# Kernel tuning notes

Measured on AMD Instinct MI355X. Metric: run time of the kernel, lower is better.

The kernel has to match this reference:

```python
import jax, jax.numpy as jnp
import numpy as np

H = 8          # num_heads
CHUNK = 68     # tokens_per_chunk = blocks_per_chunk(4) * tokens_per_block(17)
EPS = 1e-5


def _layer_norm(t, w, b):
    m = t.mean(-1, keepdims=True)
    v = t.var(-1, keepdims=True)
    return (t - m) / jnp.sqrt(v + EPS) * w + b


def _forward(tokens, embedding, Wq, bq, Wk, bk, Wv, bv, Wg, bg, Wo, bo,
             gn_w, gn_b, ln1_w, ln1_b, ln2_w, ln2_b, w1, b1, w2, b2):
    B, S = tokens.shape
    L, D, _ = Wq.shape
    dh = D // H
    n_chunks = S // CHUNK

    x = embedding[tokens]  # [B,S,D]

    # per-head decay gammas (standard RetNet)
    gamma = 1.0 - 2.0 ** (-5.0 - jnp.arange(H, dtype=jnp.float32))  # [H]

    # rotary relative-position tables (absolute positions, fresh state n=0)
    pos = jnp.arange(S, dtype=jnp.float32)
    inv = 1.0 / (10000.0 ** (jnp.arange(0, dh, 2, dtype=jnp.float32) / dh))
    ang = pos[:, None] * inv[None, :]                      # [S, dh/2]
    cs = jnp.concatenate([jnp.cos(ang)] * 2, -1)[None, :, None, :]  # [1,S,1,dh]
    sn = jnp.concatenate([jnp.sin(ang)] * 2, -1)[None, :, None, :]

    def rot(t):  # t: [B,S,H,dh]
        t1, t2 = jnp.split(t, 2, axis=-1)
        return t * cs + jnp.concatenate([-t2, t1], -1) * sn

    # chunkwise decay structures
    idx = jnp.arange(CHUNK, dtype=jnp.float32)
    expo = idx[:, None] - idx[None, :]
    Dmask = jnp.where(expo >= 0, gamma[:, None, None] ** expo[None], 0.0)  # [H,C,C]
    cross_dec = gamma[None, :] ** (idx[:, None] + 1.0)          # [C,H]
    k_dec = gamma[None, :] ** (CHUNK - 1.0 - idx[:, None])      # [C,H]
    chunk_dec = gamma ** CHUNK                                  # [H]

    for l in range(L):
        h = _layer_norm(x, ln1_w[l], ln1_b[l])
        q = rot((h @ Wq[l] + bq[l]).reshape(B, S, H, dh))
        k = rot((h @ Wk[l] + bk[l]).reshape(B, S, H, dh)) * (dh ** -0.5)
        v = (h @ Wv[l] + bv[l]).reshape(B, S, H, dh)
        # split into chunks, scan carries the per-head KV state [B,H,dh,dh]
        qc = q.reshape(B, n_chunks, CHUNK, H, dh).transpose(1, 0, 2, 3, 4)
        kc = k.reshape(B, n_chunks, CHUNK, H, dh).transpose(1, 0, 2, 3, 4)
        vc = v.reshape(B, n_chunks, CHUNK, H, dh).transpose(1, 0, 2, 3, 4)

        def step(state, qkv):
            qq, kk, vv = qkv  # each [B,C,H,dh]
            inner = jnp.einsum('bihd,bjhd->bhij', qq, kk) * Dmask
            out = jnp.einsum('bhij,bjhd->bihd', inner, vv)
            out = out + jnp.einsum('bihd,bhde->bihe', qq, state) * cross_dec[None, :, :, None]
            state = state * chunk_dec[None, :, None, None] + \
                jnp.einsum('bjhd,bjhe->bhde', kk * k_dec[None, :, :, None], vv)
            return state, out

        state0 = jnp.zeros((B, H, dh, dh), dtype=x.dtype)
        _, ret = jax.lax.scan(step, state0, (qc, kc, vc))
        ret = ret.transpose(1, 0, 2, 3, 4).reshape(B, S, H, dh)
        # per-head group norm
        m = ret.mean(-1, keepdims=True)
        vr = ret.var(-1, keepdims=True)
        ret = (ret - m) / jnp.sqrt(vr + EPS)
        ret = (ret * gn_w[l].reshape(H, dh) + gn_b[l].reshape(H, dh)).reshape(B, S, D)
        g = jax.nn.silu(h @ Wg[l] + bg[l])
        x = x + (g * ret) @ Wo[l] + bo[l]
        h2 = _layer_norm(x, ln2_w[l], ln2_b[l])
        x = x + jax.nn.silu(h2 @ w1[l] + b1[l]) @ w2[l] + b2[l]
    return x


def setup_inputs() -> dict:
    key = jax.random.key(0)
    B, S, D, L, FF, V = 16, 408, 512, 10, 2048, 519
    ks = jax.random.split(key, 16)
    r = lambda i, shape, s=0.02: jax.random.normal(ks[i], shape, dtype=jnp.float32) * s
    return {
        'tokens': jax.random.randint(ks[0], (B, S), 0, V, dtype=jnp.int32),
        'embedding': r(1, (V, D)),
        'Wq': r(2, (L, D, D)), 'bq': jnp.zeros((L, D), jnp.float32),
        'Wk': r(3, (L, D, D)), 'bk': jnp.zeros((L, D), jnp.float32),
        'Wv': r(4, (L, D, D)), 'bv': jnp.zeros((L, D), jnp.float32),
        'Wg': r(5, (L, D, D)), 'bg': jnp.zeros((L, D), jnp.float32),
        'Wo': r(6, (L, D, D)), 'bo': jnp.zeros((L, D), jnp.float32),
        'gn_w': jnp.ones((L, D), jnp.float32), 'gn_b': jnp.zeros((L, D), jnp.float32),
        'ln1_w': jnp.ones((L, D), jnp.float32), 'ln1_b': jnp.zeros((L, D), jnp.float32),
        'ln2_w': jnp.ones((L, D), jnp.float32), 'ln2_b': jnp.zeros((L, D), jnp.float32),
        'w1': r(7, (L, D, FF)), 'b1': jnp.zeros((L, FF), jnp.float32),
        'w2': r(8, (L, FF, D)), 'b2': jnp.zeros((L, D), jnp.float32),
    }


def reference(tokens, embedding, Wq, bq, Wk, bk, Wv, bv, Wg, bg, Wo, bo,
              gn_w, gn_b, ln1_w, ln1_b, ln2_w, ln2_b, w1, b1, w2, b2):
    return _forward(tokens, embedding, Wq, bq, Wk, bk, Wv, bv, Wg, bg, Wo, bo,
                    gn_w, gn_b, ln1_w, ln1_b, ln2_w, ln2_b, w1, b1, w2, b2)
```

## Files before the change

### kernel.cpp

```cpp
#include <hip/hip_runtime.h>
#include <hip/hip_bf16.h>

#define H 8
#define DH 64
#define DMODEL 512
#define SEQ 408
#define BATCH 16
#define NLAYER 10
#define FFDIM 2048
#define CHUNK 68
#define NCHUNK 6
#define M (BATCH*SEQ)
#define EPS 1e-5f

typedef __hip_bfloat16 bf16;
typedef unsigned short ushort_t;
typedef short bf8v __attribute__((ext_vector_type(8)));
typedef float f4v  __attribute__((ext_vector_type(4)));

static constexpr size_t QKVG_STRIDE = 2u*512*512;
static constexpr size_t QKVG_HL     = 512*512;
static constexpr size_t WO_HI = 0;
static constexpr size_t WO_LO = WO_HI + 512*512;
static constexpr size_t W1_HI = WO_LO + 512*512;
static constexpr size_t W1_LO = W1_HI + 2048*512;
static constexpr size_t W2_HI = W1_LO + 2048*512;
static constexpr size_t W2_LO = W2_HI + 512*2048;

__device__ __forceinline__ float us2f(unsigned short u){ return __uint_as_float(((unsigned)u) << 16); }
__device__ __forceinline__ unsigned short f2bfs(float f){
  __bf16 h = (__bf16)f;
  return *(unsigned short*)&h;
}
__device__ __forceinline__ void split2(float f, unsigned short& hi, unsigned short& lo){
  hi = f2bfs(f);
  lo = f2bfs(f - us2f(hi));
}

typedef const __attribute__((address_space(1))) unsigned int* gas_ptr;
typedef __attribute__((address_space(3))) unsigned int* las_ptr;
__device__ __forceinline__ void gld16(const void* g, void* l){
  __builtin_amdgcn_global_load_lds((gas_ptr)g, (las_ptr)l, 16, 0, 0);
}

__device__ __forceinline__ int xcd_swz(int fid, int nwg){
  int q = nwg >> 3;
  return (fid & 7) * q + (fid >> 3);
}

__global__ void embed_kernel(const int* __restrict__ tokens, const float* __restrict__ emb,
                             float* __restrict__ x){
  int idx = blockIdx.x*256 + threadIdx.x;
  if (idx >= M*DMODEL) return;
  int r = idx >> 9; int d = idx & 511;
  x[idx] = emb[(size_t)tokens[r]*DMODEL + d];
}

__global__ __launch_bounds__(256) void ln_kernel(const float* __restrict__ x,
    const float* __restrict__ w, const float* __restrict__ b,
    ushort_t* __restrict__ hhi, ushort_t* __restrict__ hlo){
  __shared__ float red[8];
  int r = blockIdx.x, tid = threadIdx.x;
  size_t base = (size_t)r*DMODEL;
  float v0 = x[base + tid], v1 = x[base + tid + 256];
  float s = v0 + v1, s2 = v0*v0 + v1*v1;
  int lane = tid & 63, wv = tid >> 6;
  #pragma unroll
  for (int o = 32; o; o >>= 1){ s += __shfl_xor(s, o); s2 += __shfl_xor(s2, o); }
  if (lane == 0){ red[wv] = s; red[wv+4] = s2; }
  __syncthreads();
  float tot  = red[0]+red[1]+red[2]+red[3];
  float tot2 = red[4]+red[5]+red[6]+red[7];
  float mean = tot * (1.0f/512.0f);
  float var  = tot2 * (1.0f/512.0f) - mean*mean;
  float rinv = rsqrtf(var + EPS);
  float o0 = (v0-mean)*rinv*w[tid]     + b[tid];
  float o1 = (v1-mean)*rinv*w[tid+256] + b[tid+256];
  unsigned short hi, lo;
  split2(o0, hi, lo); hhi[base+tid] = hi; hlo[base+tid] = lo;
  split2(o1, hi, lo); hhi[base+tid+256] = hi; hlo[base+tid+256] = lo;
}

__device__ __forceinline__ void wsplit_tile(const float* __restrict__ W,
    ushort_t* __restrict__ hi, ushort_t* __restrict__ lo,
    int N, int K, int n0, int k0)
{
  __shared__ float tb[32][33];
  int tx = threadIdx.x & 31, ty = threadIdx.x >> 5;
  #pragma unroll
  for (int r = 0; r < 32; r += 8)
    tb[ty+r][tx] = W[(size_t)(k0+ty+r)*N + n0 + tx];
  __syncthreads();
  #pragma unroll
  for (int r = 0; r < 32; r += 8){
    float v = tb[tx][ty+r];
    unsigned short h, l; split2(v, h, l);
    size_t o = (size_t)(n0+ty+r)*K + k0 + tx;
    hi[o] = h; lo[o] = l;
  }
}

__global__ __launch_bounds__(256) void wsplit_qkvg_kernel(
    const float* __restrict__ Wq, const float* __restrict__ Wk,
    const float* __restrict__ Wv, const float* __restrict__ Wg,
    ushort_t* __restrict__ wsp)
{
  int z = blockIdx.z;
  const float* W = (z==0)?Wq:(z==1)?Wk:(z==2)?Wv:Wg;
  ushort_t* hi = wsp + (size_t)z*QKVG_STRIDE;
  wsplit_tile(W, hi, hi + QKVG_HL, 512, 512, blockIdx.x*32, blockIdx.y*32);
}

__global__ __launch_bounds__(256) void wsplit_ffo_kernel(
    const float* __restrict__ Wo, const float* __restrict__ w1,
    const float* __restrict__ w2, ushort_t* __restrict__ wsp)
{
  int b = blockIdx.x;
  const float* W; ushort_t* hi; int N, K, n0, k0;
  if (b < 256){
    W = Wo; hi = wsp + WO_HI; N = 512; K = 512;
    n0 = (b & 15)*32; k0 = (b >> 4)*32;
  } else if (b < 1280){
    int bb = b - 256;
    W = w1; hi = wsp + W1_HI; N = 2048; K = 512;
    n0 = (bb & 63)*32; k0 = (bb >> 6)*32;
  } else {
    int bb = b - 1280;
    W = w2; hi = wsp + W2_HI; N = 512; K = 2048;
    n0 = (bb & 15)*32; k0 = (bb >> 4)*32;
  }
  wsplit_tile(W, hi, hi + (size_t)N*K, N, K, n0, k0);
}

#define BK 32

template<int TBN>
__global__ __launch_bounds__(256) void gemm_ps_kernel(
    const ushort_t* __restrict__ Ahi, const ushort_t* __restrict__ Alo,
    const ushort_t* __restrict__ Bhi, const ushort_t* __restrict__ Blo,
    const float* __restrict__ bias,
    const float* Cin, float* Cout, ushort_t* Co_hi, ushort_t* Co_lo,
    int N, int K, int epi)
{
  constexpr int TNW = TBN/32;
  __shared__ __align__(16) short AsH[2][64*BK];
  __shared__ __align__(16) short AsL[2][64*BK];
  __shared__ __align__(16) short BsH[2][TBN*BK];
  __shared__ __align__(16) short BsL[2][TBN*BK];
  int tid = threadIdx.x;
  int lane = tid & 63, wave = tid >> 6;
  int wm = (wave >> 1) * 32, wn = (wave & 1) * (TBN/2);
  int l15 = lane & 15, quad = lane >> 4;

  int nwg = gridDim.x * gridDim.y;
  int fid = blockIdx.y * gridDim.x + blockIdx.x;
  int swz = xcd_swz(fid, nwg);
  int bn = (swz % gridDim.x) * TBN;
  int bm = (swz / gridDim.x) * 64;

  f4v acc[2][TNW];
  #pragma unroll
  for (int i = 0; i < 2; i++)
    #pragma unroll
    for (int j = 0; j < TNW; j++) acc[i][j] = (f4v){0.f,0.f,0.f,0.f};

  int arow = tid >> 2, ak = (tid & 3) * 8;
  const ushort_t* aHp  = Ahi + (size_t)(bm + arow)*K + ak;
  const ushort_t* aLp  = Alo + (size_t)(bm + arow)*K + ak;
  const ushort_t* bHp  = Bhi + (size_t)(bn + arow)*K + ak;
  const ushort_t* bLp  = Blo + (size_t)(bn + arow)*K + ak;
  const ushort_t* bHp2 = Bhi + (size_t)(bn + 64 + arow)*K + ak;
  const ushort_t* bLp2 = Blo + (size_t)(bn + 64 + arow)*K + ak;

  auto STAGE = [&](int buf, int kofs){
    gld16(aHp + kofs, &AsH[buf][tid*8]);
    gld16(aLp + kofs, &AsL[buf][tid*8]);
    gld16(bHp + kofs, &BsH[buf][tid*8]);
    gld16(bLp + kofs, &BsL[buf][tid*8]);
    if constexpr (TBN == 128){
      gld16(bHp2 + kofs, &BsH[buf][tid*8 + 2048]);
      gld16(bLp2 + kofs, &BsL[buf][tid*8 + 2048]);
    }
  };

  STAGE(0, 0);
  STAGE(1, BK);
  const int nt = K / BK;
  for (int t = 0; t < nt; t++){
    if (t + 1 < nt){
      if constexpr (TBN == 128) asm volatile("s_waitcnt vmcnt(6)" ::: "memory");
      else                      asm volatile("s_waitcnt vmcnt(4)" ::: "memory");
    } else {
      asm volatile("s_waitcnt vmcnt(0)" ::: "memory");
    }
    __builtin_amdgcn_s_barrier();
    asm volatile("" ::: "memory");
    int cur = t & 1;
    bf8v afh[2], afl[2], bfh[TNW], bfl[TNW];
    #pragma unroll
    for (int i = 0; i < 2; i++){
      afh[i] = *(const bf8v*)&AsH[cur][(wm + i*16 + l15)*BK + quad*8];
      afl[i] = *(const bf8v*)&AsL[cur][(wm + i*16 + l15)*BK + quad*8];
    }
    #pragma unroll
    for (int j = 0; j < TNW; j++){
      bfh[j] = *(const bf8v*)&BsH[cur][(wn + j*16 + l15)*BK + quad*8];
      bfl[j] = *(const bf8v*)&BsL[cur][(wn + j*16 + l15)*BK + quad*8];
    }
    #pragma unroll
    for (int i = 0; i < 2; i++)
      #pragma unroll
      for (int j = 0; j < TNW; j++){
        acc[i][j] = __builtin_amdgcn_mfma_f32_16x16x32_bf16(afh[i], bfl[j], acc[i][j], 0, 0, 0);
        acc[i][j] = __builtin_amdgcn_mfma_f32_16x16x32_bf16(afl[i], bfh[j], acc[i][j], 0, 0, 0);
        acc[i][j] = __builtin_amdgcn_mfma_f32_16x16x32_bf16(afh[i], bfh[j], acc[i][j], 0, 0, 0);
      }
    asm volatile("s_waitcnt lgkmcnt(0)" ::: "memory");
    __builtin_amdgcn_s_barrier();
    asm volatile("" ::: "memory");
    if (t + 2 < nt) STAGE(cur, (t+2)*BK);
  }
  #pragma unroll
  for (int i = 0; i < 2; i++){
    int m0 = bm + wm + i*16 + quad*4;
    #pragma unroll
    for (int j = 0; j < TNW; j++){
      int n = bn + wn + j*16 + l15;
      float bsv = bias[n];
      #pragma unroll
      for (int r = 0; r < 4; r++){
        int m = m0 + r;
        float c = acc[i][j][r] + bsv;
        if (epi == 1) c = c / (1.0f + expf(-c));
        if (epi == 2) c += Cin[(size_t)m*N + n];
        if (Co_hi){
          unsigned short hi, lo; split2(c, hi, lo);
          Co_hi[(size_t)m*N + n] = hi;
          Co_lo[(size_t)m*N + n] = lo;
        } else {
          Cout[(size_t)m*N + n] = c;
        }
      }
    }
  }
}

__global__ __launch_bounds__(256) void gemm_qkvg_kernel(
    const ushort_t* __restrict__ Ahi, const ushort_t* __restrict__ Alo,
    const ushort_t* __restrict__ wsp,
    const float* __restrict__ bq, const float* __restrict__ bk,
    const float* __restrict__ bv, const float* __restrict__ bg,
    float* __restrict__ qo, float* __restrict__ ko,
    float* __restrict__ vo, float* __restrict__ go)
{
  const int N = DMODEL, K = DMODEL;
  __shared__ __align__(16) short AsH[2][64*BK];
  __shared__ __align__(16) short AsL[2][64*BK];
  __shared__ __align__(16) short BsH[2][128*BK];
  __shared__ __align__(16) short BsL[2][128*BK];
  int tid = threadIdx.x;
  int lane = tid & 63, wave = tid >> 6;
  int wm = (wave >> 1) * 32, wn = (wave & 1) * 64;
  int l15 = lane & 15, quad = lane >> 4;

  int nwg = gridDim.x * gridDim.y;
  int fid = blockIdx.y * gridDim.x + blockIdx.x;
  int swz = xcd_swz(fid, nwg);
  int bx = swz % gridDim.x;
  int which = bx >> 2;
  int bn = (bx & 3) * 128;
  int bm = (swz / gridDim.x) * 64;

  const ushort_t* Bhi = wsp + (size_t)which * QKVG_STRIDE;
  const ushort_t* Blo = Bhi + QKVG_HL;
  const float* bias = (which==0) ? bq : (which==1) ? bk : (which==2) ? bv : bg;
  float* out        = (which==0) ? qo : (which==1) ? ko : (which==2) ? vo : go;

  f4v acc[2][4];
  #pragma unroll
  for (int i = 0; i < 2; i++)
    #pragma unroll
    for (int j = 0; j < 4; j++) acc[i][j] = (f4v){0.f,0.f,0.f,0.f};

  int arow = tid >> 2, ak = (tid & 3) * 8;
  const ushort_t* aHp  = Ahi + (size_t)(bm + arow)*K + ak;
  const ushort_t* aLp  = Alo + (size_t)(bm + arow)*K + ak;
  const ushort_t* bHp  = Bhi + (size_t)(bn + arow)*K + ak;
  const ushort_t* bLp  = Blo + (size_t)(bn + arow)*K + ak;
  const ushort_t* bHp2 = Bhi + (size_t)(bn + 64 + arow)*K + ak;
  const ushort_t* bLp2 = Blo + (size_t)(bn + 64 + arow)*K + ak;

  auto STAGE = [&](int buf, int kofs){
    gld16(aHp + kofs, &AsH[buf][tid*8]);
    gld16(aLp + kofs, &AsL[buf][tid*8]);
    gld16(bHp + kofs, &BsH[buf][tid*8]);
    gld16(bLp + kofs, &BsL[buf][tid*8]);
    gld16(bHp2 + kofs, &BsH[buf][tid*8 + 2048]);
    gld16(bLp2 + kofs, &BsL[buf][tid*8 + 2048]);
  };

  STAGE(0, 0);
  STAGE(1, BK);
  const int nt = K / BK;
  for (int t = 0; t < nt; t++){
    if (t + 1 < nt) asm volatile("s_waitcnt vmcnt(6)" ::: "memory");
    else            asm volatile("s_waitcnt vmcnt(0)" ::: "memory");
    __builtin_amdgcn_s_barrier();
    asm volatile("" ::: "memory");
    int cur = t & 1;
    bf8v afh[2], afl[2], bfh[4], bfl[4];
    #pragma unroll
    for (int i = 0; i < 2; i++){
      afh[i] = *(const bf8v*)&AsH[cur][(wm + i*16 + l15)*BK + quad*8];
      afl[i] = *(const bf8v*)&AsL[cur][(wm + i*16 + l15)*BK + quad*8];
    }
    #pragma unroll
    for (int j = 0; j < 4; j++){
      bfh[j] = *(const bf8v*)&BsH[cur][(wn + j*16 + l15)*BK + quad*8];
      bfl[j] = *(const bf8v*)&BsL[cur][(wn + j*16 + l15)*BK + quad*8];
    }
    #pragma unroll
    for (int i = 0; i < 2; i++)
      #pragma unroll
      for (int j = 0; j < 4; j++){
        acc[i][j] = __builtin_amdgcn_mfma_f32_16x16x32_bf16(afh[i], bfl[j], acc[i][j], 0, 0, 0);
        acc[i][j] = __builtin_amdgcn_mfma_f32_16x16x32_bf16(afl[i], bfh[j], acc[i][j], 0, 0, 0);
        acc[i][j] = __builtin_amdgcn_mfma_f32_16x16x32_bf16(afh[i], bfh[j], acc[i][j], 0, 0, 0);
      }
    asm volatile("s_waitcnt lgkmcnt(0)" ::: "memory");
    __builtin_amdgcn_s_barrier();
    asm volatile("" ::: "memory");
    if (t + 2 < nt) STAGE(cur, (t+2)*BK);
  }
  #pragma unroll
  for (int i = 0; i < 2; i++){
    int m0 = bm + wm + i*16 + quad*4;
    #pragma unroll
    for (int j = 0; j < 4; j++){
      int n = bn + wn + j*16 + l15;
      float bsv = bias[n];
      #pragma unroll
      for (int r = 0; r < 4; r++){
        int m = m0 + r;
        float c = acc[i][j][r] + bsv;
        if (which == 3) c = c / (1.0f + expf(-c));
        out[(size_t)m*N + n] = c;
      }
    }
  }
}

__global__ void rope_kernel(float* __restrict__ q, float* __restrict__ k){
  int idx = blockIdx.x*256 + threadIdx.x;
  if (idx >= M*256) return;
  int r = idx >> 8, p = idx & 255;
  int hh = p >> 5, i = p & 31;
  int s = r % SEQ;
  float inv = powf(10000.0f, -(float)(2*i) * (1.0f/64.0f));
  float ang = (float)s * inv;
  float sn, c; sincosf(ang, &sn, &c);
  size_t base = (size_t)r*DMODEL + hh*64 + i;
  float q1 = q[base], q2 = q[base+32];
  q[base]    = q1*c - q2*sn;
  q[base+32] = q2*c + q1*sn;
  float k1 = k[base], k2 = k[base+32];
  const float sc = 0.125f;
  k[base]    = (k1*c - k2*sn)*sc;
  k[base+32] = (k2*c + k1*sn)*sc;
}

__global__ __launch_bounds__(256) void ret_chunkkv_kernel(
    const float* __restrict__ k, const float* __restrict__ v, float* __restrict__ Ast)
{
  __shared__ __align__(16) float kT[DH][CHUNK];
  __shared__ __align__(16) float vs[CHUNK][DH];
  __shared__ float gpw[CHUNK];
  int tid = threadIdx.x;
  int c = blockIdx.x % NCHUNK;
  int bh = blockIdx.x / NCHUNK;
  int hh = bh & 7, b = bh >> 3;
  float gamma = 1.0f - exp2f(-5.0f - (float)hh);
  if (tid < CHUNK) gpw[tid] = powf(gamma, (float)(CHUNK-1-tid));
  size_t rowbase = ((size_t)(b*SEQ + c*CHUNK))*DMODEL + hh*DH;
  for (int e = tid; e < CHUNK*DH; e += 256){
    int i = e >> 6, d = e & 63;
    size_t g = rowbase + (size_t)i*DMODEL + d;
    kT[d][i] = k[g];
    vs[i][d] = v[g];
  }
  __syncthreads();
  float* A = Ast + (size_t)blockIdx.x * (DH*DH);
  for (int e = tid; e < DH*16; e += 256){
    int d = e >> 4, q4 = (e & 15) * 4;
    float4 a4 = {0,0,0,0};
    for (int j = 0; j < CHUNK; j++){
      float kj = kT[d][j] * gpw[j];
      float4 v4 = *(const float4*)&vs[j][q4];
      a4.x += kj*v4.x; a4.y += kj*v4.y; a4.z += kj*v4.z; a4.w += kj*v4.w;
    }
    *(float4*)&A[d*DH + q4] = a4;
  }
}

__global__ __launch_bounds__(256) void ret_scan_kernel(float* __restrict__ Ast)
{
  int bh = blockIdx.x, hh = bh & 7;
  float gamma = 1.0f - exp2f(-5.0f - (float)hh);
  float chdec = powf(gamma, (float)CHUNK);
  int tid = threadIdx.x;
  float4 run[4];
  #pragma unroll
  for (int t = 0; t < 4; t++) run[t] = (float4){0,0,0,0};
  size_t base = (size_t)bh * NCHUNK * (DH*DH) + (size_t)tid*16;
  for (int c = 0; c < NCHUNK; c++){
    float4* slot = (float4*)(Ast + base + (size_t)c*(DH*DH));
    float4 a[4];
    #pragma unroll
    for (int t = 0; t < 4; t++) a[t] = slot[t];
    #pragma unroll
    for (int t = 0; t < 4; t++) slot[t] = run[t];
    #pragma unroll
    for (int t = 0; t < 4; t++){
      run[t].x = run[t].x*chdec + a[t].x;
      run[t].y = run[t].y*chdec + a[t].y;
      run[t].z = run[t].z*chdec + a[t].z;
      run[t].w = run[t].w*chdec + a[t].w;
    }
  }
}

__global__ __launch_bounds__(256) void ret_out_kernel(
    const float* __restrict__ q, const float* __restrict__ k, const float* __restrict__ v,
    const float* __restrict__ Ast, float* __restrict__ ret)
{
  __shared__ __align__(16) float qs[CHUNK][DH];
  __shared__ __align__(16) float kT[DH][CHUNK];
  __shared__ __align__(16) float vs[CHUNK][DH];
  __shared__ __align__(16) float sts[DH*DH];
  __shared__ float inner[34][CHUNK];
  __shared__ float gpw[CHUNK];
  int tid = threadIdx.x;
  int c = blockIdx.x % NCHUNK;
  int bh = blockIdx.x / NCHUNK;
  int hh = bh & 7, b = bh >> 3;
  float gamma = 1.0f - exp2f(-5.0f - (float)hh);
  if (tid < CHUNK) gpw[tid] = powf(gamma, (float)tid);
  size_t rowbase = ((size_t)(b*SEQ + c*CHUNK))*DMODEL + hh*DH;
  for (int e = tid; e < CHUNK*DH; e += 256){
    int i = e >> 6, d = e & 63;
    size_t g = rowbase + (size_t)i*DMODEL + d;
    qs[i][d] = q[g];
    kT[d][i] = k[g];
    vs[i][d] = v[g];
  }
  const float* st = Ast + (size_t)blockIdx.x * (DH*DH);
  for (int e = tid*4; e < DH*DH; e += 1024)
    *(float4*)&sts[e] = *(const float4*)&st[e];
  __syncthreads();
  for (int p = 0; p < 2; p++){
    int i0 = p*34;
    for (int e = tid; e < 34*CHUNK; e += 256){
      int ii = e / CHUNK, j = e - ii*CHUNK;
      int i = i0 + ii;
      float val = 0.0f;
      if (j <= i){
        float dot = 0.0f;
        #pragma unroll 16
        for (int d = 0; d < DH; d++) dot += qs[i][d] * kT[d][j];
        val = dot * gpw[i-j];
      }
      inner[ii][j] = val;
    }
    __syncthreads();
    for (int e = tid; e < 34*16; e += 256){
      int ii = e >> 4, q4 = (e & 15) * 4;
      int i = i0 + ii;
      float4 o4 = {0,0,0,0};
      for (int j = 0; j <= i; j++){
        float w = inner[ii][j];
        float4 v4 = *(const float4*)&vs[j][q4];
        o4.x += w*v4.x; o4.y += w*v4.y; o4.z += w*v4.z; o4.w += w*v4.w;
      }
      float4 c4 = {0,0,0,0};
      #pragma unroll 8
      for (int e2 = 0; e2 < DH; e2++){
        float qv = qs[i][e2];
        float4 s4 = *(const float4*)&sts[e2*DH + q4];
        c4.x += qv*s4.x; c4.y += qv*s4.y; c4.z += qv*s4.z; c4.w += qv*s4.w;
      }
      float cd = gpw[i] * gamma;
      size_t ob = rowbase + (size_t)i*DMODEL + q4;
      float4 o; o.x = o4.x + cd*c4.x; o.y = o4.y + cd*c4.y;
      o.z = o4.z + cd*c4.z; o.w = o4.w + cd*c4.w;
      *(float4*)&ret[ob] = o;
    }
    __syncthreads();
  }
}

__global__ __launch_bounds__(512) void gnorm_gate_kernel(const float* __restrict__ ret,
    const float* __restrict__ g, const float* __restrict__ gnw, const float* __restrict__ gnb,
    ushort_t* __restrict__ ohi, ushort_t* __restrict__ olo)
{
  int r = blockIdx.x, tid = threadIdx.x;
  size_t idx = (size_t)r*DMODEL + tid;
  float val = ret[idx];
  float s = val, s2 = val*val;
  #pragma unroll
  for (int o = 32; o; o >>= 1){ s += __shfl_xor(s, o); s2 += __shfl_xor(s2, o); }
  float mean = s * (1.0f/64.0f);
  float var  = s2 * (1.0f/64.0f) - mean*mean;
  float y = (val - mean) * rsqrtf(var + EPS);
  y = y * gnw[tid] + gnb[tid];
  y = y * g[idx];
  unsigned short hi, lo; split2(y, hi, lo);
  ohi[idx] = hi; olo[idx] = lo;
}

__global__ void outwrite_kernel(const float* __restrict__ x, float* __restrict__ out){
  int idx = blockIdx.x*256 + threadIdx.x;
  if (idx < M*DMODEL) out[idx] = x[idx];
}

extern "C" void kernel_launch(void* const* d_in, const int* in_sizes, int n_in,
                              void* d_out, int out_size, void* d_ws, size_t ws_size,
                              hipStream_t stream)
{
  (void)in_sizes; (void)n_in; (void)out_size; (void)ws_size;
  const int*   tokens = (const int*)d_in[0];
  const float* emb  = (const float*)d_in[1];
  const float* Wq = (const float*)d_in[2];  const float* bq = (const float*)d_in[3];
  const float* Wk = (const float*)d_in[4];  const float* bk = (const float*)d_in[5];
  const float* Wv = (const float*)d_in[6];  const float* bv = (const float*)d_in[7];
  const float* Wg = (const float*)d_in[8];  const float* bg = (const float*)d_in[9];
  const float* Wo = (const float*)d_in[10]; const float* bo = (const float*)d_in[11];
  const float* gnw = (const float*)d_in[12]; const float* gnb = (const float*)d_in[13];
  const float* ln1w = (const float*)d_in[14]; const float* ln1b = (const float*)d_in[15];
  const float* ln2w = (const float*)d_in[16]; const float* ln2b = (const float*)d_in[17];
  const float* w1 = (const float*)d_in[18]; const float* b1 = (const float*)d_in[19];
  const float* w2 = (const float*)d_in[20]; const float* b2 = (const float*)d_in[21];

  const size_t MD = (size_t)M*DMODEL;
  float* xf = (float*)d_ws;
  float* qf = xf + MD;
  float* kf = qf + MD;
  float* vf = kf + MD;
  float* gf = vf + MD;
  float* rf = gf + MD;
  ushort_t* h_hi = (ushort_t*)(rf + MD);
  ushort_t* h_lo = h_hi + MD;
  float* Ast = (float*)h_hi;
  ushort_t* rg_hi = h_hi;
  ushort_t* rg_lo = h_lo;
  ushort_t* ff_hi = (ushort_t*)qf;
  ushort_t* ff_lo = (ushort_t*)vf;
  ushort_t* wsp = (ushort_t*)rf;

  embed_kernel<<<(M*DMODEL)/256, 256, 0, stream>>>(tokens, emb, xf);

  dim3 gqkvg(16, M/64);
  dim3 g512(DMODEL/64, M/64);
  dim3 gff(FFDIM/128, M/64);
  dim3 gsplit4(16, 16, 4);
  for (int l = 0; l < NLAYER; l++){
    const size_t wO = (size_t)l*DMODEL*DMODEL;
    const size_t bO = (size_t)l*DMODEL;
    const size_t w1O = (size_t)l*DMODEL*FFDIM;
    const size_t b1O = (size_t)l*FFDIM;
    wsplit_qkvg_kernel<<<gsplit4, 256, 0, stream>>>(Wq + wO, Wk + wO, Wv + wO, Wg + wO, wsp);
    ln_kernel<<<M, 256, 0, stream>>>(xf, ln1w + bO, ln1b + bO, h_hi, h_lo);
    gemm_qkvg_kernel<<<gqkvg, 256, 0, stream>>>(h_hi, h_lo, wsp,
        bq + bO, bk + bO, bv + bO, bg + bO,
        qf, kf, vf, gf);
    rope_kernel<<<M, 256, 0, stream>>>(qf, kf);
    ret_chunkkv_kernel<<<BATCH*H*NCHUNK, 256, 0, stream>>>(kf, vf, Ast);
    ret_scan_kernel<<<BATCH*H, 256, 0, stream>>>(Ast);
    ret_out_kernel<<<BATCH*H*NCHUNK, 256, 0, stream>>>(qf, kf, vf, Ast, rf);
    gnorm_gate_kernel<<<M, 512, 0, stream>>>(rf, gf, gnw + bO, gnb + bO, rg_hi, rg_lo);
    wsplit_ffo_kernel<<<2304, 256, 0, stream>>>(Wo + wO, w1 + w1O, w2 + w1O, wsp);
    gemm_ps_kernel<64><<<g512, 256, 0, stream>>>(rg_hi, rg_lo,
        wsp + WO_HI, wsp + WO_LO, bo + bO, xf, xf, nullptr, nullptr, DMODEL, DMODEL, 2);
    ln_kernel<<<M, 256, 0, stream>>>(xf, ln2w + bO, ln2b + bO, h_hi, h_lo);
    gemm_ps_kernel<128><<<gff, 256, 0, stream>>>(h_hi, h_lo,
        wsp + W1_HI, wsp + W1_LO, b1 + b1O, nullptr, nullptr, ff_hi, ff_lo, FFDIM, DMODEL, 1);
    gemm_ps_kernel<64><<<g512, 256, 0, stream>>>(ff_hi, ff_lo,
        wsp + W2_HI, wsp + W2_LO, b2 + bO, xf, xf, nullptr, nullptr, DMODEL, FFDIM, 2);
  }
  outwrite_kernel<<<(M*DMODEL)/256, 256, 0, stream>>>(xf, (float*)d_out);
}
```

Baseline: 3.747 ms.

## Use triple-buffered XOR-swizzled interleaved hi/lo LDS tiles in split-bf16 GEMMs

Both split-bf16 GEMM kernels now stage the hi and lo halves of A and B into a single interleaved LDS tile per buffer, using an XOR swizzle on 16-byte chunks to avoid bank conflicts on the fragment reads. The double buffer becomes a triple buffer, so the next prefetch is issued right after the top barrier. This removes the second barrier and lgkmcnt wait at the end of each k-step. The cost is more LDS per block, which can reduce occupancy, plus extra address arithmetic in the staging loop.

```diff
diff --git a/kernel.cpp b/kernel.cpp
--- a/kernel.cpp
+++ b/kernel.cpp
@@ -143,10 +143,9 @@
     int N, int K, int epi)
 {
   constexpr int TNW = TBN/32;
-  __shared__ __align__(16) short AsH[2][64*BK];
-  __shared__ __align__(16) short AsL[2][64*BK];
-  __shared__ __align__(16) short BsH[2][TBN*BK];
-  __shared__ __align__(16) short BsL[2][TBN*BK];
+  constexpr int BSLOT = TBN*8/256;
+  __shared__ __align__(16) short AsF[3][64*64];
+  __shared__ __align__(16) short BsF[3][TBN*64];
   int tid = threadIdx.x;
   int lane = tid & 63, wave = tid >> 6;
   int wm = (wave >> 1) * 32, wn = (wave & 1) * (TBN/2);
@@ -164,22 +163,22 @@
     #pragma unroll
     for (int j = 0; j < TNW; j++) acc[i][j] = (f4v){0.f,0.f,0.f,0.f};
 
-  int arow = tid >> 2, ak = (tid & 3) * 8;
-  const ushort_t* aHp  = Ahi + (size_t)(bm + arow)*K + ak;
-  const ushort_t* aLp  = Alo + (size_t)(bm + arow)*K + ak;
-  const ushort_t* bHp  = Bhi + (size_t)(bn + arow)*K + ak;
-  const ushort_t* bLp  = Blo + (size_t)(bn + arow)*K + ak;
-  const ushort_t* bHp2 = Bhi + (size_t)(bn + 64 + arow)*K + ak;
-  const ushort_t* bLp2 = Blo + (size_t)(bn + 64 + arow)*K + ak;
-
   auto STAGE = [&](int buf, int kofs){
-    gld16(aHp + kofs, &AsH[buf][tid*8]);
-    gld16(aLp + kofs, &AsL[buf][tid*8]);
-    gld16(bHp + kofs, &BsH[buf][tid*8]);
-    gld16(bLp + kofs, &BsL[buf][tid*8]);
-    if constexpr (TBN == 128){
-      gld16(bHp2 + kofs, &BsH[buf][tid*8 + 2048]);
-      gld16(bLp2 + kofs, &BsL[buf][tid*8 + 2048]);
+    #pragma unroll
+    for (int s = 0; s < 2; s++){
+      int slot = tid + s*256;
+      int r = slot >> 3, d = slot & 7;
+      int c = d ^ (r & 7);
+      const ushort_t* src = (c & 1) ? Alo : Ahi;
+      gld16(src + (size_t)(bm + r)*K + kofs + (c >> 1)*8, &AsF[buf][slot*8]);
+    }
+    #pragma unroll
+    for (int s = 0; s < BSLOT; s++){
+      int slot = tid + s*256;
+      int r = slot >> 3, d = slot & 7;
+      int c = d ^ (r & 7);
+      const ushort_t* src = (c & 1) ? Blo : Bhi;
+      gld16(src + (size_t)(bn + r)*K + kofs + (c >> 1)*8, &BsF[buf][slot*8]);
     }
   };
 
@@ -195,17 +194,20 @@
     }
     __builtin_amdgcn_s_barrier();
     asm volatile("" ::: "memory");
-    int cur = t & 1;
+    if (t + 2 < nt) STAGE((t + 2) % 3, (t + 2)*BK);
+    int cur = t % 3;
     bf8v afh[2], afl[2], bfh[TNW], bfl[TNW];
     #pragma unroll
     for (int i = 0; i < 2; i++){
-      afh[i] = *(const bf8v*)&AsH[cur][(wm + i*16 + l15)*BK + quad*8];
-      afl[i] = *(const bf8v*)&AsL[cur][(wm + i*16 + l15)*BK + quad*8];
+      int r = wm + i*16 + l15;
+      afh[i] = *(const bf8v*)&AsF[cur][r*64 + (((2*quad)   ^ (r&7))*8)];
+      afl[i] = *(const bf8v*)&AsF[cur][r*64 + (((2*quad+1) ^ (r&7))*8)];
     }
     #pragma unroll
     for (int j = 0; j < TNW; j++){
-      bfh[j] = *(const bf8v*)&BsH[cur][(wn + j*16 + l15)*BK + quad*8];
-      bfl[j] = *(const bf8v*)&BsL[cur][(wn + j*16 + l15)*BK + quad*8];
+      int r = wn + j*16 + l15;
+      bfh[j] = *(const bf8v*)&BsF[cur][r*64 + (((2*quad)   ^ (r&7))*8)];
+      bfl[j] = *(const bf8v*)&BsF[cur][r*64 + (((2*quad+1) ^ (r&7))*8)];
     }
     #pragma unroll
     for (int i = 0; i < 2; i++)
@@ -215,10 +217,6 @@
         acc[i][j] = __builtin_amdgcn_mfma_f32_16x16x32_bf16(afl[i], bfh[j], acc[i][j], 0, 0, 0);
         acc[i][j] = __builtin_amdgcn_mfma_f32_16x16x32_bf16(afh[i], bfh[j], acc[i][j], 0, 0, 0);
       }
-    asm volatile("s_waitcnt lgkmcnt(0)" ::: "memory");
-    __builtin_amdgcn_s_barrier();
-    asm volatile("" ::: "memory");
-    if (t + 2 < nt) STAGE(cur, (t+2)*BK);
   }
   #pragma unroll
   for (int i = 0; i < 2; i++){
@@ -254,10 +252,8 @@
     float* __restrict__ vo, float* __restrict__ go)
 {
   const int N = DMODEL, K = DMODEL;
-  __shared__ __align__(16) short AsH[2][64*BK];
-  __shared__ __align__(16) short AsL[2][64*BK];
-  __shared__ __align__(16) short BsH[2][128*BK];
-  __shared__ __align__(16) short BsL[2][128*BK];
+  __shared__ __align__(16) short AsF[3][64*64];
+  __shared__ __align__(16) short BsF[3][128*64];
   int tid = threadIdx.x;
   int lane = tid & 63, wave = tid >> 6;
   int wm = (wave >> 1) * 32, wn = (wave & 1) * 64;
@@ -282,21 +278,23 @@
     #pragma unroll
     for (int j = 0; j < 4; j++) acc[i][j] = (f4v){0.f,0.f,0.f,0.f};
 
-  int arow = tid >> 2, ak = (tid & 3) * 8;
-  const ushort_t* aHp  = Ahi + (size_t)(bm + arow)*K + ak;
-  const ushort_t* aLp  = Alo + (size_t)(bm + arow)*K + ak;
-  const ushort_t* bHp  = Bhi + (size_t)(bn + arow)*K + ak;
-  const ushort_t* bLp  = Blo + (size_t)(bn + arow)*K + ak;
-  const ushort_t* bHp2 = Bhi + (size_t)(bn + 64 + arow)*K + ak;
-  const ushort_t* bLp2 = Blo + (size_t)(bn + 64 + arow)*K + ak;
-
   auto STAGE = [&](int buf, int kofs){
-    gld16(aHp + kofs, &AsH[buf][tid*8]);
-    gld16(aLp + kofs, &AsL[buf][tid*8]);
-    gld16(bHp + kofs, &BsH[buf][tid*8]);
-    gld16(bLp + kofs, &BsL[buf][tid*8]);
-    gld16(bHp2 + kofs, &BsH[buf][tid*8 + 2048]);
-    gld16(bLp2 + kofs, &BsL[buf][tid*8 + 2048]);
+    #pragma unroll
+    for (int s = 0; s < 2; s++){
+      int slot = tid + s*256;
+      int r = slot >> 3, d = slot & 7;
+      int c = d ^ (r & 7);
+      const ushort_t* src = (c & 1) ? Alo : Ahi;
+      gld16(src + (size_t)(bm + r)*K + kofs + (c >> 1)*8, &AsF[buf][slot*8]);
+    }
+    #pragma unroll
+    for (int s = 0; s < 4; s++){
+      int slot = tid + s*256;
+      int r = slot >> 3, d = slot & 7;
+      int c = d ^ (r & 7);
+      const ushort_t* src = (c & 1) ? Blo : Bhi;
+      gld16(src + (size_t)(bn + r)*K + kofs + (c >> 1)*8, &BsF[buf][slot*8]);
+    }
   };
 
   STAGE(0, 0);
@@ -307,17 +305,20 @@
     else            asm volatile("s_waitcnt vmcnt(0)" ::: "memory");
     __builtin_amdgcn_s_barrier();
     asm volatile("" ::: "memory");
-    int cur = t & 1;
+    if (t + 2 < nt) STAGE((t + 2) % 3, (t + 2)*BK);
+    int cur = t % 3;
     bf8v afh[2], afl[2], bfh[4], bfl[4];
     #pragma unroll
     for (int i = 0; i < 2; i++){
-      afh[i] = *(const bf8v*)&AsH[cur][(wm + i*16 + l15)*BK + quad*8];
-      afl[i] = *(const bf8v*)&AsL[cur][(wm + i*16 + l15)*BK + quad*8];
+      int r = wm + i*16 + l15;
+      afh[i] = *(const bf8v*)&AsF[cur][r*64 + (((2*quad)   ^ (r&7))*8)];
+      afl[i] = *(const bf8v*)&AsF[cur][r*64 + (((2*quad+1) ^ (r&7))*8)];
     }
     #pragma unroll
     for (int j = 0; j < 4; j++){
-      bfh[j] = *(const bf8v*)&BsH[cur][(wn + j*16 + l15)*BK + quad*8];
-      bfl[j] = *(const bf8v*)&BsL[cur][(wn + j*16 + l15)*BK + quad*8];
+      int r = wn + j*16 + l15;
+      bfh[j] = *(const bf8v*)&BsF[cur][r*64 + (((2*quad)   ^ (r&7))*8)];
+      bfl[j] = *(const bf8v*)&BsF[cur][r*64 + (((2*quad+1) ^ (r&7))*8)];
     }
     #pragma unroll
     for (int i = 0; i < 2; i++)
@@ -327,10 +328,6 @@
         acc[i][j] = __builtin_amdgcn_mfma_f32_16x16x32_bf16(afl[i], bfh[j], acc[i][j], 0, 0, 0);
         acc[i][j] = __builtin_amdgcn_mfma_f32_16x16x32_bf16(afh[i], bfh[j], acc[i][j], 0, 0, 0);
       }
-    asm volatile("s_waitcnt lgkmcnt(0)" ::: "memory");
-    __builtin_amdgcn_s_barrier();
-    asm volatile("" ::: "memory");
-    if (t + 2 < nt) STAGE(cur, (t+2)*BK);
   }
   #pragma unroll
   for (int i = 0; i < 2; i++){
```

New measurement: 4.504 ms. +20.2%, slower.

## Load GEMM B operand directly from global and triple-buffer A tiles

Applied to the files above, without the earlier changes.

Both bf16x3 split-precision GEMM kernels stop staging the B (weight) tiles through shared memory. Each wave now reads its MFMA B fragments straight from global memory into registers every k-step. The A tiles move to a three-slot LDS ring, which allows a single barrier per iteration with the next stage issued right after it. The aim is to cut LDS traffic and one barrier per k-step. In exchange, B loads are issued and consumed in the same iteration with no prefetch, so global latency may be exposed and waves sharing B columns fetch the same data twice. Correctness depends on the fixed vmcnt(2) wait interacting properly with the compiler's own waits.

```diff
diff --git a/kernel.cpp b/kernel.cpp
--- a/kernel.cpp
+++ b/kernel.cpp
@@ -143,10 +143,8 @@
     int N, int K, int epi)
 {
   constexpr int TNW = TBN/32;
-  __shared__ __align__(16) short AsH[2][64*BK];
-  __shared__ __align__(16) short AsL[2][64*BK];
-  __shared__ __align__(16) short BsH[2][TBN*BK];
-  __shared__ __align__(16) short BsL[2][TBN*BK];
+  __shared__ __align__(16) short AsH[3][64*BK];
+  __shared__ __align__(16) short AsL[3][64*BK];
   int tid = threadIdx.x;
   int lane = tid & 63, wave = tid >> 6;
   int wm = (wave >> 1) * 32, wn = (wave & 1) * (TBN/2);
@@ -165,47 +163,42 @@
     for (int j = 0; j < TNW; j++) acc[i][j] = (f4v){0.f,0.f,0.f,0.f};
 
   int arow = tid >> 2, ak = (tid & 3) * 8;
-  const ushort_t* aHp  = Ahi + (size_t)(bm + arow)*K + ak;
-  const ushort_t* aLp  = Alo + (size_t)(bm + arow)*K + ak;
-  const ushort_t* bHp  = Bhi + (size_t)(bn + arow)*K + ak;
-  const ushort_t* bLp  = Blo + (size_t)(bn + arow)*K + ak;
-  const ushort_t* bHp2 = Bhi + (size_t)(bn + 64 + arow)*K + ak;
-  const ushort_t* bLp2 = Blo + (size_t)(bn + 64 + arow)*K + ak;
+  const ushort_t* aHp = Ahi + (size_t)(bm + arow)*K + ak;
+  const ushort_t* aLp = Alo + (size_t)(bm + arow)*K + ak;
+  const ushort_t* bHp[TNW];
+  const ushort_t* bLp[TNW];
+  #pragma unroll
+  for (int j = 0; j < TNW; j++){
+    size_t ro = (size_t)(bn + wn + j*16 + l15)*K + quad*8;
+    bHp[j] = Bhi + ro;
+    bLp[j] = Blo + ro;
+  }
 
   auto STAGE = [&](int buf, int kofs){
     gld16(aHp + kofs, &AsH[buf][tid*8]);
     gld16(aLp + kofs, &AsL[buf][tid*8]);
-    gld16(bHp + kofs, &BsH[buf][tid*8]);
-    gld16(bLp + kofs, &BsL[buf][tid*8]);
-    if constexpr (TBN == 128){
-      gld16(bHp2 + kofs, &BsH[buf][tid*8 + 2048]);
-      gld16(bLp2 + kofs, &BsL[buf][tid*8 + 2048]);
-    }
   };
 
   STAGE(0, 0);
   STAGE(1, BK);
   const int nt = K / BK;
   for (int t = 0; t < nt; t++){
-    if (t + 1 < nt){
-      if constexpr (TBN == 128) asm volatile("s_waitcnt vmcnt(6)" ::: "memory");
-      else                      asm volatile("s_waitcnt vmcnt(4)" ::: "memory");
-    } else {
-      asm volatile("s_waitcnt vmcnt(0)" ::: "memory");
-    }
+    asm volatile("s_waitcnt vmcnt(2)" ::: "memory");
     __builtin_amdgcn_s_barrier();
     asm volatile("" ::: "memory");
-    int cur = t & 1;
-    bf8v afh[2], afl[2], bfh[TNW], bfl[TNW];
+    if (t + 2 < nt) STAGE((t + 2) % 3, (t + 2)*BK);
+    int cur = t % 3;
+    bf8v bfh[TNW], bfl[TNW];
+    #pragma unroll
+    for (int j = 0; j < TNW; j++){
+      bfh[j] = *(const bf8v*)(bHp[j] + t*BK);
+      bfl[j] = *(const bf8v*)(bLp[j] + t*BK);
+    }
+    bf8v afh[2], afl[2];
     #pragma unroll
     for (int i = 0; i < 2; i++){
       afh[i] = *(const bf8v*)&AsH[cur][(wm + i*16 + l15)*BK + quad*8];
       afl[i] = *(const bf8v*)&AsL[cur][(wm + i*16 + l15)*BK + quad*8];
-    }
-    #pragma unroll
-    for (int j = 0; j < TNW; j++){
-      bfh[j] = *(const bf8v*)&BsH[cur][(wn + j*16 + l15)*BK + quad*8];
-      bfl[j] = *(const bf8v*)&BsL[cur][(wn + j*16 + l15)*BK + quad*8];
     }
     #pragma unroll
     for (int i = 0; i < 2; i++)
@@ -215,10 +208,6 @@
         acc[i][j] = __builtin_amdgcn_mfma_f32_16x16x32_bf16(afl[i], bfh[j], acc[i][j], 0, 0, 0);
         acc[i][j] = __builtin_amdgcn_mfma_f32_16x16x32_bf16(afh[i], bfh[j], acc[i][j], 0, 0, 0);
       }
-    asm volatile("s_waitcnt lgkmcnt(0)" ::: "memory");
-    __builtin_amdgcn_s_barrier();
-    asm volatile("" ::: "memory");
-    if (t + 2 < nt) STAGE(cur, (t+2)*BK);
   }
   #pragma unroll
   for (int i = 0; i < 2; i++){
@@ -254,10 +243,8 @@
     float* __restrict__ vo, float* __restrict__ go)
 {
   const int N = DMODEL, K = DMODEL;
-  __shared__ __align__(16) short AsH[2][64*BK];
-  __shared__ __align__(16) short AsL[2][64*BK];
-  __shared__ __align__(16) short BsH[2][128*BK];
-  __shared__ __align__(16) short BsL[2][128*BK];
+  __shared__ __align__(16) short AsH[3][64*BK];
+  __shared__ __align__(16) short AsL[3][64*BK];
   int tid = threadIdx.x;
   int lane = tid & 63, wave = tid >> 6;
   int wm = (wave >> 1) * 32, wn = (wave & 1) * 64;
@@ -283,41 +270,42 @@
     for (int j = 0; j < 4; j++) acc[i][j] = (f4v){0.f,0.f,0.f,0.f};
 
   int arow = tid >> 2, ak = (tid & 3) * 8;
-  const ushort_t* aHp  = Ahi + (size_t)(bm + arow)*K + ak;
-  const ushort_t* aLp  = Alo + (size_t)(bm + arow)*K + ak;
-  const ushort_t* bHp  = Bhi + (size_t)(bn + arow)*K + ak;
-  const ushort_t* bLp  = Blo + (size_t)(bn + arow)*K + ak;
-  const ushort_t* bHp2 = Bhi + (size_t)(bn + 64 + arow)*K + ak;
-  const ushort_t* bLp2 = Blo + (size_t)(bn + 64 + arow)*K + ak;
+  const ushort_t* aHp = Ahi + (size_t)(bm + arow)*K + ak;
+  const ushort_t* aLp = Alo + (size_t)(bm + arow)*K + ak;
+  const ushort_t* bHp[4];
+  const ushort_t* bLp[4];
+  #pragma unroll
+  for (int j = 0; j < 4; j++){
+    size_t ro = (size_t)(bn + wn + j*16 + l15)*K + quad*8;
+    bHp[j] = Bhi + ro;
+    bLp[j] = Blo + ro;
+  }
 
   auto STAGE = [&](int buf, int kofs){
     gld16(aHp + kofs, &AsH[buf][tid*8]);
     gld16(aLp + kofs, &AsL[buf][tid*8]);
-    gld16(bHp + kofs, &BsH[buf][tid*8]);
-    gld16(bLp + kofs, &BsL[buf][tid*8]);
-    gld16(bHp2 + kofs, &BsH[buf][tid*8 + 2048]);
-    gld16(bLp2 + kofs, &BsL[buf][tid*8 + 2048]);
   };
 
   STAGE(0, 0);
   STAGE(1, BK);
   const int nt = K / BK;
   for (int t = 0; t < nt; t++){
-    if (t + 1 < nt) asm volatile("s_waitcnt vmcnt(6)" ::: "memory");
-    else            asm volatile("s_waitcnt vmcnt(0)" ::: "memory");
+    asm volatile("s_waitcnt vmcnt(2)" ::: "memory");
     __builtin_amdgcn_s_barrier();
     asm volatile("" ::: "memory");
-    int cur = t & 1;
-    bf8v afh[2], afl[2], bfh[4], bfl[4];
+    if (t + 2 < nt) STAGE((t + 2) % 3, (t + 2)*BK);
+    int cur = t % 3;
+    bf8v bfh[4], bfl[4];
+    #pragma unroll
+    for (int j = 0; j < 4; j++){
+      bfh[j] = *(const bf8v*)(bHp[j] + t*BK);
+      bfl[j] = *(const bf8v*)(bLp[j] + t*BK);
+    }
+    bf8v afh[2], afl[2];
     #pragma unroll
     for (int i = 0; i < 2; i++){
       afh[i] = *(const bf8v*)&AsH[cur][(wm + i*16 + l15)*BK + quad*8];
       afl[i] = *(const bf8v*)&AsL[cur][(wm + i*16 + l15)*BK + quad*8];
-    }
-    #pragma unroll
-    for (int j = 0; j < 4; j++){
-      bfh[j] = *(const bf8v*)&BsH[cur][(wn + j*16 + l15)*BK + quad*8];
-      bfl[j] = *(const bf8v*)&BsL[cur][(wn + j*16 + l15)*BK + quad*8];
     }
     #pragma unroll
     for (int i = 0; i < 2; i++)
@@ -327,10 +315,6 @@
         acc[i][j] = __builtin_amdgcn_mfma_f32_16x16x32_bf16(afl[i], bfh[j], acc[i][j], 0, 0, 0);
         acc[i][j] = __builtin_amdgcn_mfma_f32_16x16x32_bf16(afh[i], bfh[j], acc[i][j], 0, 0, 0);
       }
-    asm volatile("s_waitcnt lgkmcnt(0)" ::: "memory");
-    __builtin_amdgcn_s_barrier();
-    asm volatile("" ::: "memory");
-    if (t + 2 < nt) STAGE(cur, (t+2)*BK);
   }
   #pragma unroll
   for (int i = 0; i < 2; i++){
```

Measured after the change: 5.508 ms. 47.0% more time.

## Split-K the FFN down-projection with atomics and shrink GEMM N-tiles to 64

Applied to the files above, without the earlier changes.

The W2 GEMM (K=2048) is split four ways along K using gridDim.z, and each slice atomically adds its partial into the residual stream, with the bias added only by the first slice. The QKVG and FF1 GEMMs move from 128-wide to 64-wide N tiles, which doubles the number of workgroups. Both changes aim to fill more CUs, since each GEMM only had a few hundred tiles to spread across the device. In exchange there is more operand reloading, float atomic traffic, and a summation order that is no longer deterministic.

```diff
diff --git a/kernel.cpp b/kernel.cpp
--- a/kernel.cpp
+++ b/kernel.cpp
@@ -157,6 +157,8 @@
   int swz = xcd_swz(fid, nwg);
   int bn = (swz % gridDim.x) * TBN;
   int bm = (swz / gridDim.x) * 64;
+  int Kloc = K / gridDim.z;
+  int k0 = blockIdx.z * Kloc;
 
   f4v acc[2][TNW];
   #pragma unroll
@@ -165,12 +167,12 @@
     for (int j = 0; j < TNW; j++) acc[i][j] = (f4v){0.f,0.f,0.f,0.f};
 
   int arow = tid >> 2, ak = (tid & 3) * 8;
-  const ushort_t* aHp  = Ahi + (size_t)(bm + arow)*K + ak;
-  const ushort_t* aLp  = Alo + (size_t)(bm + arow)*K + ak;
-  const ushort_t* bHp  = Bhi + (size_t)(bn + arow)*K + ak;
-  const ushort_t* bLp  = Blo + (size_t)(bn + arow)*K + ak;
-  const ushort_t* bHp2 = Bhi + (size_t)(bn + 64 + arow)*K + ak;
-  const ushort_t* bLp2 = Blo + (size_t)(bn + 64 + arow)*K + ak;
+  const ushort_t* aHp  = Ahi + (size_t)(bm + arow)*K + k0 + ak;
+  const ushort_t* aLp  = Alo + (size_t)(bm + arow)*K + k0 + ak;
+  const ushort_t* bHp  = Bhi + (size_t)(bn + arow)*K + k0 + ak;
+  const ushort_t* bLp  = Blo + (size_t)(bn + arow)*K + k0 + ak;
+  const ushort_t* bHp2 = Bhi + (size_t)(bn + 64 + arow)*K + k0 + ak;
+  const ushort_t* bLp2 = Blo + (size_t)(bn + 64 + arow)*K + k0 + ak;
 
   auto STAGE = [&](int buf, int kofs){
     gld16(aHp + kofs, &AsH[buf][tid*8]);
@@ -185,7 +187,7 @@
 
   STAGE(0, 0);
   STAGE(1, BK);
-  const int nt = K / BK;
+  const int nt = Kloc / BK;
   for (int t = 0; t < nt; t++){
     if (t + 1 < nt){
       if constexpr (TBN == 128) asm volatile("s_waitcnt vmcnt(6)" ::: "memory");
@@ -230,6 +232,11 @@
       #pragma unroll
       for (int r = 0; r < 4; r++){
         int m = m0 + r;
+        if (epi == 3){
+          float c = acc[i][j][r] + (blockIdx.z == 0 ? bsv : 0.0f);
+          atomicAdd(&Cout[(size_t)m*N + n], c);
+          continue;
+        }
         float c = acc[i][j][r] + bsv;
         if (epi == 1) c = c / (1.0f + expf(-c));
         if (epi == 2) c += Cin[(size_t)m*N + n];
@@ -256,19 +263,19 @@
   const int N = DMODEL, K = DMODEL;
   __shared__ __align__(16) short AsH[2][64*BK];
   __shared__ __align__(16) short AsL[2][64*BK];
-  __shared__ __align__(16) short BsH[2][128*BK];
-  __shared__ __align__(16) short BsL[2][128*BK];
+  __shared__ __align__(16) short BsH[2][64*BK];
+  __shared__ __align__(16) short BsL[2][64*BK];
   int tid = threadIdx.x;
   int lane = tid & 63, wave = tid >> 6;
-  int wm = (wave >> 1) * 32, wn = (wave & 1) * 64;
+  int wm = (wave >> 1) * 32, wn = (wave & 1) * 32;
   int l15 = lane & 15, quad = lane >> 4;
 
   int nwg = gridDim.x * gridDim.y;
   int fid = blockIdx.y * gridDim.x + blockIdx.x;
   int swz = xcd_swz(fid, nwg);
   int bx = swz % gridDim.x;
-  int which = bx >> 2;
-  int bn = (bx & 3) * 128;
+  int which = bx >> 3;
+  int bn = (bx & 7) * 64;
   int bm = (swz / gridDim.x) * 64;
 
   const ushort_t* Bhi = wsp + (size_t)which * QKVG_STRIDE;
@@ -276,53 +283,46 @@
   const float* bias = (which==0) ? bq : (which==1) ? bk : (which==2) ? bv : bg;
   float* out        = (which==0) ? qo : (which==1) ? ko : (which==2) ? vo : go;
 
-  f4v acc[2][4];
+  f4v acc[2][2];
   #pragma unroll
   for (int i = 0; i < 2; i++)
     #pragma unroll
-    for (int j = 0; j < 4; j++) acc[i][j] = (f4v){0.f,0.f,0.f,0.f};
+    for (int j = 0; j < 2; j++) acc[i][j] = (f4v){0.f,0.f,0.f,0.f};
 
   int arow = tid >> 2, ak = (tid & 3) * 8;
-  const ushort_t* aHp  = Ahi + (size_t)(bm + arow)*K + ak;
-  const ushort_t* aLp  = Alo + (size_t)(bm + arow)*K + ak;
-  const ushort_t* bHp  = Bhi + (size_t)(bn + arow)*K + ak;
-  const ushort_t* bLp  = Blo + (size_t)(bn + arow)*K + ak;
-  const ushort_t* bHp2 = Bhi + (size_t)(bn + 64 + arow)*K + ak;
-  const ushort_t* bLp2 = Blo + (size_t)(bn + 64 + arow)*K + ak;
+  const ushort_t* aHp = Ahi + (size_t)(bm + arow)*K + ak;
+  const ushort_t* aLp = Alo + (size_t)(bm + arow)*K + ak;
+  const ushort_t* bHp = Bhi + (size_t)(bn + arow)*K + ak;
+  const ushort_t* bLp = Blo + (size_t)(bn + arow)*K + ak;
 
   auto STAGE = [&](int buf, int kofs){
     gld16(aHp + kofs, &AsH[buf][tid*8]);
     gld16(aLp + kofs, &AsL[buf][tid*8]);
     gld16(bHp + kofs, &BsH[buf][tid*8]);
     gld16(bLp + kofs, &BsL[buf][tid*8]);
-    gld16(bHp2 + kofs, &BsH[buf][tid*8 + 2048]);
-    gld16(bLp2 + kofs, &BsL[buf][tid*8 + 2048]);
   };
 
   STAGE(0, 0);
   STAGE(1, BK);
   const int nt = K / BK;
   for (int t = 0; t < nt; t++){
-    if (t + 1 < nt) asm volatile("s_waitcnt vmcnt(6)" ::: "memory");
+    if (t + 1 < nt) asm volatile("s_waitcnt vmcnt(4)" ::: "memory");
     else            asm volatile("s_waitcnt vmcnt(0)" ::: "memory");
     __builtin_amdgcn_s_barrier();
     asm volatile("" ::: "memory");
     int cur = t & 1;
-    bf8v afh[2], afl[2], bfh[4], bfl[4];
+    bf8v afh[2], afl[2], bfh[2], bfl[2];
     #pragma unroll
     for (int i = 0; i < 2; i++){
       afh[i] = *(const bf8v*)&AsH[cur][(wm + i*16 + l15)*BK + quad*8];
       afl[i] = *(const bf8v*)&AsL[cur][(wm + i*16 + l15)*BK + quad*8];
-    }
-    #pragma unroll
-    for (int j = 0; j < 4; j++){
-      bfh[j] = *(const bf8v*)&BsH[cur][(wn + j*16 + l15)*BK + quad*8];
-      bfl[j] = *(const bf8v*)&BsL[cur][(wn + j*16 + l15)*BK + quad*8];
+      bfh[i] = *(const bf8v*)&BsH[cur][(wn + i*16 + l15)*BK + quad*8];
+      bfl[i] = *(const bf8v*)&BsL[cur][(wn + i*16 + l15)*BK + quad*8];
     }
     #pragma unroll
     for (int i = 0; i < 2; i++)
       #pragma unroll
-      for (int j = 0; j < 4; j++){
+      for (int j = 0; j < 2; j++){
         acc[i][j] = __builtin_amdgcn_mfma_f32_16x16x32_bf16(afh[i], bfl[j], acc[i][j], 0, 0, 0);
         acc[i][j] = __builtin_amdgcn_mfma_f32_16x16x32_bf16(afl[i], bfh[j], acc[i][j], 0, 0, 0);
         acc[i][j] = __builtin_amdgcn_mfma_f32_16x16x32_bf16(afh[i], bfh[j], acc[i][j], 0, 0, 0);
@@ -336,7 +336,7 @@
   for (int i = 0; i < 2; i++){
     int m0 = bm + wm + i*16 + quad*4;
     #pragma unroll
-    for (int j = 0; j < 4; j++){
+    for (int j = 0; j < 2; j++){
       int n = bn + wn + j*16 + l15;
       float bsv = bias[n];
       #pragma unroll
@@ -558,9 +558,10 @@
 
   embed_kernel<<<(M*DMODEL)/256, 256, 0, stream>>>(tokens, emb, xf);
 
-  dim3 gqkvg(16, M/64);
+  dim3 gqkvg(32, M/64);
   dim3 g512(DMODEL/64, M/64);
-  dim3 gff(FFDIM/128, M/64);
+  dim3 gff(FFDIM/64, M/64);
+  dim3 gw2(DMODEL/64, M/64, 4);
   dim3 gsplit4(16, 16, 4);
   for (int l = 0; l < NLAYER; l++){
     const size_t wO = (size_t)l*DMODEL*DMODEL;
@@ -581,10 +582,10 @@
     gemm_ps_kernel<64><<<g512, 256, 0, stream>>>(rg_hi, rg_lo,
         wsp + WO_HI, wsp + WO_LO, bo + bO, xf, xf, nullptr, nullptr, DMODEL, DMODEL, 2);
     ln_kernel<<<M, 256, 0, stream>>>(xf, ln2w + bO, ln2b + bO, h_hi, h_lo);
-    gemm_ps_kernel<128><<<gff, 256, 0, stream>>>(h_hi, h_lo,
+    gemm_ps_kernel<64><<<gff, 256, 0, stream>>>(h_hi, h_lo,
         wsp + W1_HI, wsp + W1_LO, b1 + b1O, nullptr, nullptr, ff_hi, ff_lo, FFDIM, DMODEL, 1);
-    gemm_ps_kernel<64><<<g512, 256, 0, stream>>>(ff_hi, ff_lo,
-        wsp + W2_HI, wsp + W2_LO, b2 + bO, xf, xf, nullptr, nullptr, DMODEL, FFDIM, 2);
+    gemm_ps_kernel<64><<<gw2, 256, 0, stream>>>(ff_hi, ff_lo,
+        wsp + W2_HI, wsp + W2_LO, b2 + bO, nullptr, xf, nullptr, nullptr, DMODEL, FFDIM, 3);
   }
   outwrite_kernel<<<(M*DMODEL)/256, 256, 0, stream>>>(xf, (float*)d_out);
 }
```

After: 3.691 ms. No clear change (-1.5%).
